# Optimization experiments

Measured on AMD Instinct MI355X. Metric: run time of the kernel, lower is better.

Reference implementation:

```python
import jax, jax.numpy as jnp
import numpy as np

N = 100000   # nodes
P = 3        # metapaths
E = 800000   # edges per metapath (avg degree 8)
IN = 128     # in_size
H = 4        # layer_num_heads
D = 32       # out_size per head
HID = 64     # semantic attention hidden
NEG_SLOPE = 0.2


def setup_inputs() -> dict:
    key = jax.random.key(0)
    ks = jax.random.split(key, 10)
    h = jax.random.normal(ks[0], (N, IN), jnp.float32)
    edge_src = jax.random.randint(ks[1], (P, E), 0, N, dtype=jnp.int32).astype(jnp.int64)
    edge_dst = jax.random.randint(ks[2], (P, E), 0, N, dtype=jnp.int32).astype(jnp.int64)
    W = jax.random.normal(ks[3], (P, IN, H * D), jnp.float32) * 0.05
    attn_l = jax.random.normal(ks[4], (P, H, D), jnp.float32) * 0.05
    attn_r = jax.random.normal(ks[5], (P, H, D), jnp.float32) * 0.05
    bias = jnp.zeros((P, H * D), jnp.float32)
    sa_w1 = jax.random.normal(ks[6], (H * D, HID), jnp.float32) * 0.05
    sa_b1 = jnp.zeros((HID,), jnp.float32)
    sa_w2 = jax.random.normal(ks[7], (HID, 1), jnp.float32) * 0.05
    return {"h": h, "edge_src": edge_src, "edge_dst": edge_dst, "W": W,
            "attn_l": attn_l, "attn_r": attn_r, "bias": bias,
            "sa_w1": sa_w1, "sa_b1": sa_b1, "sa_w2": sa_w2}


def _gat_conv(h, src, dst, Wp, al, ar, bp):
    # DGL GATConv: project, per-edge additive attention, edge softmax over dst, scatter-sum.
    n = h.shape[0]
    feat = (h @ Wp).reshape(n, H, D)              # [N,H,D]
    el = (feat * al).sum(-1)                      # [N,H]
    er = (feat * ar).sum(-1)                      # [N,H]
    e = jax.nn.leaky_relu(el[src] + er[dst], NEG_SLOPE)   # [E,H]
    emax = jax.ops.segment_max(e, dst, num_segments=n)    # [N,H]
    emax = jnp.where(jnp.isfinite(emax), emax, 0.0)       # zero-in-degree guard
    ex = jnp.exp(e - emax[dst])                            # [E,H]
    denom = jax.ops.segment_sum(ex, dst, num_segments=n)   # [N,H]
    alpha = ex / jnp.maximum(denom[dst], 1e-9)              # [E,H]
    msg = alpha[:, :, None] * feat[src]                     # [E,H,D]
    out = jax.ops.segment_sum(msg, dst, num_segments=n)     # [N,H,D]
    return out.reshape(n, H * D) + bp


def reference(h, edge_src, edge_dst, W, attn_l, attn_r, bias, sa_w1, sa_b1, sa_w2):
    embs = []
    for p in range(P):  # small fixed metapath set
        embs.append(_gat_conv(h, edge_src[p], edge_dst[p], W[p], attn_l[p], attn_r[p], bias[p]))
    z = jnp.stack(embs, axis=1)                 # [N,P,H*D]
    # SemanticAttention: MLP score, mean over nodes, softmax over metapaths
    w = (jnp.tanh(z @ sa_w1 + sa_b1) @ sa_w2).mean(0)   # [P,1]
    beta = jax.nn.softmax(w, axis=0)                     # [P,1]
    return (beta[None, :, :] * z).sum(1)                 # [N,H*D]
```

## Files before the change

kernel.cpp:

```cpp
#include <hip/hip_runtime.h>
#include <hip/hip_bf16.h>
#include <math.h>

#define NN 100000
#define NP 3
#define NE 800000
#define NH 4
#define ND 32
#define HD 128
#define NHID 64

#define SLW 256
#define SBK 512
#define GB 391
#define NBLK 196
#define ECHUNK 4096
#define EPT 16
#define EMAX 2560

typedef __attribute__((ext_vector_type(8))) short short8;
typedef __attribute__((ext_vector_type(4))) float f32x4;

__device__ __forceinline__ unsigned short f2bf(float f) {
  union { float f; unsigned int u; } v; v.f = f;
  unsigned int r = v.u + 0x7FFFu + ((v.u >> 16) & 1u);
  return (unsigned short)(r >> 16);
}
__device__ __forceinline__ float bf2f(unsigned short u) {
  return __uint_as_float(((unsigned int)u) << 16);
}
__device__ __forceinline__ float tanh_fast(float x) {
  return 1.f - 2.f / (1.f + __expf(2.f * x));
}

__global__ __launch_bounds__(256) void prep_fill_kernel(
    const float* __restrict__ h, const float* __restrict__ W, const float* __restrict__ W1,
    const int* __restrict__ src_all, const int* __restrict__ dst_all,
    unsigned short* __restrict__ hb, unsigned short* __restrict__ WT,
    unsigned short* __restrict__ W1T, float* __restrict__ s,
    int* __restrict__ cntA, int* __restrict__ baseA, int* __restrict__ pairs) {
  __shared__ int hist[SBK];
  __shared__ int scanb[SBK];
  const int tid = threadIdx.x;
  const int bx = blockIdx.x;
  if (bx < 12500) {
    int i = bx * 256 + tid;
    if (i < NN * 32) {
      float4 v = ((const float4*)h)[i];
      ushort4 o;
      o.x = f2bf(v.x); o.y = f2bf(v.y); o.z = f2bf(v.z); o.w = f2bf(v.w);
      ((ushort4*)hb)[i] = o;
    }
    if (i < NP * 128 * 128) {
      int p = i >> 14, r = i & 16383, n = r >> 7, k = r & 127;
      WT[i] = f2bf(W[(size_t)p * 16384 + k * 128 + n]);
    }
    if (i < NHID * 128) {
      int n = i >> 7, k = i & 127;
      W1T[i] = f2bf(W1[(size_t)k * NHID + n]);
    }
    if (i < 4) s[i] = 0.f;
    return;
  }
  const int b2 = bx - 12500;
  const int p = b2 / NBLK, blk = b2 % NBLK;
  const int* dstp = dst_all + (size_t)p * NE;
  const int* srcp = src_all + (size_t)p * NE;
  hist[tid] = 0; hist[tid + 256] = 0;
  __syncthreads();
  int dv[EPT], sv[EPT];
#pragma unroll
  for (int k = 0; k < EPT; ++k) {
    int e = blk * ECHUNK + k * 256 + tid;
    dv[k] = -1; sv[k] = 0;
    if (e < NE) {
      dv[k] = __builtin_nontemporal_load(dstp + e);
      sv[k] = __builtin_nontemporal_load(srcp + e);
    }
    if (dv[k] >= 0) atomicAdd(&hist[(unsigned)dv[k] >> 8], 1);
  }
  __syncthreads();
  scanb[tid] = hist[tid]; scanb[tid + 256] = hist[tid + 256];
  __syncthreads();
  for (int off = 1; off < SBK; off <<= 1) {
    int a0 = (tid >= off) ? scanb[tid - off] : 0;
    int a1 = scanb[tid + 256 - off];
    __syncthreads();
    scanb[tid] += a0; scanb[tid + 256] += a1;
    __syncthreads();
  }
  int c0 = hist[tid], c1 = hist[tid + 256];
  int b0 = scanb[tid] - c0, b1 = scanb[tid + 256] - c1;
  int* cA = cntA + ((size_t)p * NBLK + blk) * SBK;
  int* bA = baseA + ((size_t)p * NBLK + blk) * SBK;
  cA[tid] = c0; cA[tid + 256] = c1;
  bA[tid] = b0; bA[tid + 256] = b1;
  __syncthreads();
  scanb[tid] = b0; scanb[tid + 256] = b1;
  hist[tid] = 0; hist[tid + 256] = 0;
  __syncthreads();
  int* prp = pairs + (size_t)p * NE + (size_t)blk * ECHUNK;
#pragma unroll
  for (int k = 0; k < EPT; ++k) {
    if (dv[k] >= 0) {
      int sl = (unsigned)dv[k] >> 8;
      int pos = scanb[sl] + atomicAdd(&hist[sl], 1);
      prp[pos] = ((dv[k] & 255) << 17) | sv[k];
    }
  }
}

__global__ __launch_bounds__(256) void gemm_mfma_kernel(
    const unsigned short* __restrict__ hb, const unsigned short* __restrict__ WT_all,
    const float* __restrict__ al_all, const float* __restrict__ ar_all,
    unsigned short* __restrict__ featb_all, float* __restrict__ el_all,
    float* __restrict__ er_all) {
  __shared__ unsigned short Bs[128 * 128];
  const int p = blockIdx.y;
  const unsigned short* WTp = WT_all + (size_t)p * 16384;
#pragma unroll
  for (int it = 0; it < 8; ++it)
    ((float4*)Bs)[it * 256 + threadIdx.x] = ((const float4*)WTp)[it * 256 + threadIdx.x];
  __syncthreads();

  const int wid = threadIdx.x >> 6, lane = threadIdx.x & 63;
  const int c = lane & 15, q = lane >> 4;
  const int tile = blockIdx.x * 4 + wid;
  const int tc = tile < 6250 ? tile : 6249;

  f32x4 acc[8];
#pragma unroll
  for (int t = 0; t < 8; ++t) acc[t] = (f32x4){0.f, 0.f, 0.f, 0.f};

  const unsigned short* arow = hb + (size_t)(tc * 16 + c) * 128 + q * 8;
#pragma unroll
  for (int kc = 0; kc < 4; ++kc) {
    short8 a = *(const short8*)(arow + kc * 32);
#pragma unroll
    for (int t = 0; t < 8; ++t) {
      short8 b = *(const short8*)(Bs + (size_t)(t * 16 + c) * 128 + kc * 32 + q * 8);
      acc[t] = __builtin_amdgcn_mfma_f32_16x16x32_bf16(a, b, acc[t], 0, 0, 0);
    }
  }
  if (tile >= 6250) return;

  unsigned short* featb = featb_all + (size_t)p * NN * 128;
#pragma unroll
  for (int t = 0; t < 8; ++t)
#pragma unroll
    for (int i = 0; i < 4; ++i)
      featb[(size_t)(tc * 16 + q * 4 + i) * 128 + t * 16 + c] = f2bf(acc[t][i]);

  const float* al = al_all + p * 128;
  const float* ar = ar_all + p * 128;
  float alv[8], arv[8];
#pragma unroll
  for (int t = 0; t < 8; ++t) { alv[t] = al[t * 16 + c]; arv[t] = ar[t * 16 + c]; }
  float elp[4][4], erp[4][4];
#pragma unroll
  for (int i = 0; i < 4; ++i)
#pragma unroll
    for (int hh = 0; hh < 4; ++hh) {
      elp[i][hh] = acc[2 * hh][i] * alv[2 * hh] + acc[2 * hh + 1][i] * alv[2 * hh + 1];
      erp[i][hh] = acc[2 * hh][i] * arv[2 * hh] + acc[2 * hh + 1][i] * arv[2 * hh + 1];
    }
#pragma unroll
  for (int m = 1; m <= 8; m <<= 1)
#pragma unroll
    for (int i = 0; i < 4; ++i)
#pragma unroll
      for (int hh = 0; hh < 4; ++hh) {
        elp[i][hh] += __shfl_xor(elp[i][hh], m);
        erp[i][hh] += __shfl_xor(erp[i][hh], m);
      }
  if (c == 0) {
    float* el = el_all + (size_t)p * NN * 4;
    float* er = er_all + (size_t)p * NN * 4;
#pragma unroll
    for (int i = 0; i < 4; ++i) {
      int row = tc * 16 + q * 4 + i;
      *(float4*)(el + (size_t)row * 4) = make_float4(elp[i][0], elp[i][1], elp[i][2], elp[i][3]);
      *(float4*)(er + (size_t)row * 4) = make_float4(erp[i][0], erp[i][1], erp[i][2], erp[i][3]);
    }
  }
}

__global__ __launch_bounds__(512) void gather2_kernel(
    const unsigned short* __restrict__ featb_all, const float* __restrict__ el_all,
    const float* __restrict__ er_all, const int* __restrict__ cntA,
    const int* __restrict__ baseA, const int* __restrict__ pairs,
    const float* __restrict__ bias_all, unsigned short* __restrict__ zb) {
  __shared__ int scnt[NBLK];
  __shared__ int sbase[NBLK];
  __shared__ int scum[NBLK];
  __shared__ int totE;
  __shared__ int hist[SLW];
  __shared__ int start[SLW];
  __shared__ int wcur[SLW];
  __shared__ int earr[EMAX];
  __shared__ int srt[EMAX];
  const int tid = threadIdx.x;
  const int p = blockIdx.y, sl = blockIdx.x;

  for (int b = tid; b < NBLK; b += 512) {
    scnt[b] = cntA[((size_t)p * NBLK + b) * SBK + sl];
    sbase[b] = baseA[((size_t)p * NBLK + b) * SBK + sl];
  }
  if (tid < SLW) hist[tid] = 0;
  __syncthreads();
  if (tid < NBLK) scum[tid] = scnt[tid];
  __syncthreads();
  for (int off = 1; off < NBLK; off <<= 1) {
    int a = (tid < NBLK && tid >= off) ? scum[tid - off] : 0;
    __syncthreads();
    if (tid < NBLK) scum[tid] += a;
    __syncthreads();
  }
  if (tid == NBLK - 1) { int t = scum[NBLK - 1]; totE = t > EMAX ? EMAX : t; }
  int excl = (tid < NBLK) ? scum[tid] - scnt[tid] : 0;
  __syncthreads();
  if (tid < NBLK) scum[tid] = excl;
  __syncthreads();
  const int total = totE;
  const int* prp = pairs + (size_t)p * NE;
  for (int e = tid; e < total; e += 512) {
    int lo = 0, hi = NBLK - 1;
    while (lo < hi) { int mid = (lo + hi + 1) >> 1; if (scum[mid] <= e) lo = mid; else hi = mid - 1; }
    int pk = prp[(size_t)lo * ECHUNK + sbase[lo] + (e - scum[lo])];
    earr[e] = pk;
    atomicAdd(&hist[pk >> 17], 1);
  }
  __syncthreads();
  if (tid < SLW) start[tid] = hist[tid];
  __syncthreads();
  for (int off = 1; off < SLW; off <<= 1) {
    int a = (tid < SLW && tid >= off) ? start[tid - off] : 0;
    __syncthreads();
    if (tid < SLW) start[tid] += a;
    __syncthreads();
  }
  if (tid < SLW) { int st = start[tid] - hist[tid]; start[tid] = st; wcur[tid] = st; }
  __syncthreads();
  for (int e = tid; e < total; e += 512) {
    int pk = earr[e];
    int pos = atomicAdd(&wcur[pk >> 17], 1);
    srt[pos] = pk & 0x1FFFF;
  }
  __syncthreads();

  const unsigned short* featb = featb_all + (size_t)p * NN * 128;
  const float* el = el_all + (size_t)p * NN * 4;
  const int w = tid >> 6, lane = tid & 63;
  const int j16 = lane & 15, hgrp = lane >> 4;
  const int sub = lane >> 4, c16 = lane & 15;
  const int hh = c16 >> 2;
  for (int nl = w; nl < SLW; nl += 8) {
    int n = sl * SLW + nl;
    if (n >= NN) continue;
    int deg = hist[nl];
    int st = start[nl];
    float4 ern = *(const float4*)(er_all + (size_t)p * NN * 4 + (size_t)n * 4);
    const float ernh = hgrp == 0 ? ern.x : hgrp == 1 ? ern.y : hgrp == 2 ? ern.z : ern.w;
    float acc[8] = {0.f, 0.f, 0.f, 0.f, 0.f, 0.f, 0.f, 0.f};
    float dsum = 0.f;
    for (int b = 0; b < deg; b += 16) {
      int s = 0; float x = 0.f;
      int jj = b + j16;
      if (jj < deg) {
        s = srt[st + jj];
        float ev = el[(size_t)s * 4 + hgrp];
        float e = ev + ernh; e = fmaxf(e, 0.2f * e);
        x = __expf(e);
      }
      int bend = deg - b; bend = bend > 16 ? 16 : bend;
      for (int i = 0; i < bend; i += 8) {
        int j0 = i + sub, j1 = i + 4 + sub;
        int s0 = __shfl(s, j0);
        int s1 = __shfl(s, j1);
        float xv0 = __shfl(x, (hh << 4) | j0);
        float xv1 = __shfl(x, (hh << 4) | j1);
        short8 f0 = *(const short8*)(featb + (size_t)s0 * 128 + c16 * 8);
        short8 f1 = *(const short8*)(featb + (size_t)s1 * 128 + c16 * 8);
        dsum += xv0 + xv1;
#pragma unroll
        for (int k = 0; k < 8; ++k) acc[k] += xv0 * bf2f((unsigned short)f0[k]);
#pragma unroll
        for (int k = 0; k < 8; ++k) acc[k] += xv1 * bf2f((unsigned short)f1[k]);
      }
    }
    dsum += __shfl_xor(dsum, 16); dsum += __shfl_xor(dsum, 32);
#pragma unroll
    for (int k = 0; k < 8; ++k) {
      acc[k] += __shfl_xor(acc[k], 16);
      acc[k] += __shfl_xor(acc[k], 32);
    }
    if (sub == 0) {
      float rd = dsum > 0.f ? 1.f / dsum : 0.f;
      const float* bias = bias_all + p * 128 + c16 * 8;
      float4 b0 = *(const float4*)(bias);
      float4 b1 = *(const float4*)(bias + 4);
      short8 o;
      o[0] = f2bf(acc[0] * rd + b0.x); o[1] = f2bf(acc[1] * rd + b0.y);
      o[2] = f2bf(acc[2] * rd + b0.z); o[3] = f2bf(acc[3] * rd + b0.w);
      o[4] = f2bf(acc[4] * rd + b1.x); o[5] = f2bf(acc[5] * rd + b1.y);
      o[6] = f2bf(acc[6] * rd + b1.z); o[7] = f2bf(acc[7] * rd + b1.w);
      *(short8*)(zb + (size_t)n * (NP * 128) + p * 128 + c16 * 8) = o;
    }
  }
}

__global__ __launch_bounds__(256) void sem_mfma_kernel(
    const unsigned short* __restrict__ zb, const unsigned short* __restrict__ W1T,
    const float* __restrict__ b1, const float* __restrict__ w2,
    float* __restrict__ s) {
  __shared__ float red3[3];
  if (threadIdx.x < 3) red3[threadIdx.x] = 0.f;
  __syncthreads();
  const int wid = threadIdx.x >> 6, lane = threadIdx.x & 63;
  const int tile = blockIdx.x * 4 + wid;
  const bool active = tile < 18750;
  const int tc = active ? tile : 18749;
  const int c = lane & 15, q = lane >> 4;
  f32x4 acc[4];
#pragma unroll
  for (int t = 0; t < 4; ++t) acc[t] = (f32x4){0.f, 0.f, 0.f, 0.f};

  const unsigned short* arow = zb + (size_t)(tc * 16 + c) * 128 + q * 8;
  const unsigned short* brow = W1T + (size_t)c * 128 + q * 8;
#pragma unroll
  for (int kc = 0; kc < 4; ++kc) {
    short8 a = *(const short8*)(arow + kc * 32);
#pragma unroll
    for (int t = 0; t < 4; ++t) {
      short8 b = *(const short8*)(brow + (size_t)t * 16 * 128 + kc * 32);
      acc[t] = __builtin_amdgcn_mfma_f32_16x16x32_bf16(a, b, acc[t], 0, 0, 0);
    }
  }
  float part[4] = {0.f, 0.f, 0.f, 0.f};
#pragma unroll
  for (int t = 0; t < 4; ++t) {
    float bb = b1[t * 16 + c], ww = w2[t * 16 + c];
#pragma unroll
    for (int i = 0; i < 4; ++i) part[i] += tanh_fast(acc[t][i] + bb) * ww;
  }
#pragma unroll
  for (int m = 1; m <= 8; m <<= 1)
#pragma unroll
    for (int i = 0; i < 4; ++i) part[i] += __shfl_xor(part[i], m);
  if (active && c == 0) {
#pragma unroll
    for (int i = 0; i < 4; ++i)
      atomicAdd(&red3[(tc * 16 + q * 4 + i) % 3], part[i]);
  }
  __syncthreads();
  if (threadIdx.x < 3) atomicAdd(&s[threadIdx.x], red3[threadIdx.x]);
}

__global__ __launch_bounds__(256) void final_kernel(
    const unsigned short* __restrict__ zb, const float* __restrict__ s,
    float* __restrict__ out) {
  int i = blockIdx.x * blockDim.x + threadIdx.x;
  if (i >= NN * 16) return;
  float w0 = s[0] * (1.f / NN), w1 = s[1] * (1.f / NN), w2c = s[2] * (1.f / NN);
  float m = fmaxf(w0, fmaxf(w1, w2c));
  float e0 = __expf(w0 - m), e1 = __expf(w1 - m), e2 = __expf(w2c - m);
  float inv = 1.f / (e0 + e1 + e2);
  float b0 = e0 * inv, b1 = e1 * inv, b2 = e2 * inv;
  int n = i >> 4, g = i & 15;
  const unsigned short* zr = zb + (size_t)n * (NP * 128) + g * 8;
  ushort4 u0a = *(const ushort4*)(zr);
  ushort4 u0b = *(const ushort4*)(zr + 4);
  ushort4 u1a = *(const ushort4*)(zr + 128);
  ushort4 u1b = *(const ushort4*)(zr + 132);
  ushort4 u2a = *(const ushort4*)(zr + 256);
  ushort4 u2b = *(const ushort4*)(zr + 260);
  float4 oa, ob;
  oa.x = b0 * bf2f(u0a.x) + b1 * bf2f(u1a.x) + b2 * bf2f(u2a.x);
  oa.y = b0 * bf2f(u0a.y) + b1 * bf2f(u1a.y) + b2 * bf2f(u2a.y);
  oa.z = b0 * bf2f(u0a.z) + b1 * bf2f(u1a.z) + b2 * bf2f(u2a.z);
  oa.w = b0 * bf2f(u0a.w) + b1 * bf2f(u1a.w) + b2 * bf2f(u2a.w);
  ob.x = b0 * bf2f(u0b.x) + b1 * bf2f(u1b.x) + b2 * bf2f(u2b.x);
  ob.y = b0 * bf2f(u0b.y) + b1 * bf2f(u1b.y) + b2 * bf2f(u2b.y);
  ob.z = b0 * bf2f(u0b.z) + b1 * bf2f(u1b.z) + b2 * bf2f(u2b.z);
  ob.w = b0 * bf2f(u0b.w) + b1 * bf2f(u1b.w) + b2 * bf2f(u2b.w);
  float* op = out + (size_t)n * 128 + g * 8;
  *(float4*)op = oa;
  *(float4*)(op + 4) = ob;
}

extern "C" void kernel_launch(void* const* d_in, const int* in_sizes, int n_in,
                              void* d_out, int out_size, void* d_ws, size_t ws_size,
                              hipStream_t stream) {
  const float* h    = (const float*)d_in[0];
  const int*   esrc = (const int*)d_in[1];
  const int*   edst = (const int*)d_in[2];
  const float* W    = (const float*)d_in[3];
  const float* al   = (const float*)d_in[4];
  const float* ar   = (const float*)d_in[5];
  const float* bias = (const float*)d_in[6];
  const float* w1   = (const float*)d_in[7];
  const float* b1   = (const float*)d_in[8];
  const float* w2   = (const float*)d_in[9];
  float* out = (float*)d_out;

  unsigned short* zb    = (unsigned short*)d_ws;
  unsigned short* featb = zb + (size_t)38400000;
  unsigned short* WT    = featb + (size_t)38400000;
  unsigned short* W1T   = WT + 49152;
  float* el   = (float*)(W1T + 8192);
  float* er   = el + (size_t)NP * NN * 4;
  float* s    = er + (size_t)NP * NN * 4;
  int* cntA  = (int*)(s + 16);
  int* baseA = cntA + (size_t)NP * NBLK * SBK;
  int* pairs = baseA + (size_t)NP * NBLK * SBK;
  unsigned short* hb = (unsigned short*)(pairs + (size_t)NP * NE);

  prep_fill_kernel<<<12500 + NP * NBLK, 256, 0, stream>>>(
      h, W, w1, esrc, edst, hb, WT, W1T, s, cntA, baseA, pairs);

  dim3 gemmGrid(NN / 64 + 1, NP);
  gemm_mfma_kernel<<<gemmGrid, 256, 0, stream>>>(hb, WT, al, ar, featb, el, er);

  dim3 g2Grid(GB, NP);
  gather2_kernel<<<g2Grid, 512, 0, stream>>>(featb, el, er, cntA, baseA, pairs, bias, zb);

  sem_mfma_kernel<<<(18750 + 3) / 4, 256, 0, stream>>>(zb, W1T, b1, w2, s);
  final_kernel<<<(NN * 16 + 255) / 256, 256, 0, stream>>>(zb, s, out);
}
```

Before: 474.7 us.

## Split gather into CSR build, edge-weight precompute, and per-node gather kernels

The fused gather kernel, which bucket-sorted edges in shared memory and then aggregated, is split into three kernels. One builds per-slice sorted edge lists and row indices in global memory, one computes exp attention weights per edge for all heads, and one does the per-destination-node feature gather with one wave per node across a much larger grid. This removes the large shared-memory footprint that limited occupancy in the gather phase, and the CSR build is placed before the GEMM. In exchange it adds global-memory round trips for the sorted edges and weights, two extra launches, and a lower EMAX cap that could truncate edges in dense slices.

```diff
diff --git a/kernel.cpp b/kernel.cpp
--- a/kernel.cpp
+++ b/kernel.cpp
@@ -16,7 +16,7 @@
 #define NBLK 196
 #define ECHUNK 4096
 #define EPT 16
-#define EMAX 2560
+#define EMAX 2368
 
 typedef __attribute__((ext_vector_type(8))) short short8;
 typedef __attribute__((ext_vector_type(4))) float f32x4;
@@ -185,11 +185,10 @@
   }
 }
 
-__global__ __launch_bounds__(512) void gather2_kernel(
-    const unsigned short* __restrict__ featb_all, const float* __restrict__ el_all,
-    const float* __restrict__ er_all, const int* __restrict__ cntA,
-    const int* __restrict__ baseA, const int* __restrict__ pairs,
-    const float* __restrict__ bias_all, unsigned short* __restrict__ zb) {
+__global__ __launch_bounds__(512) void fillB2a_kernel(
+    const int* __restrict__ cntA, const int* __restrict__ baseA,
+    const int* __restrict__ pairs, int* __restrict__ srtpk,
+    int2* __restrict__ rowidx, int* __restrict__ btot) {
   __shared__ int scnt[NBLK];
   __shared__ int sbase[NBLK];
   __shared__ int scum[NBLK];
@@ -198,9 +197,9 @@
   __shared__ int start[SLW];
   __shared__ int wcur[SLW];
   __shared__ int earr[EMAX];
-  __shared__ int srt[EMAX];
   const int tid = threadIdx.x;
   const int p = blockIdx.y, sl = blockIdx.x;
+  const size_t base = ((size_t)p * GB + sl) * EMAX;
 
   for (int b = tid; b < NBLK; b += 512) {
     scnt[b] = cntA[((size_t)p * NBLK + b) * SBK + sl];
@@ -244,68 +243,99 @@
   for (int e = tid; e < total; e += 512) {
     int pk = earr[e];
     int pos = atomicAdd(&wcur[pk >> 17], 1);
-    srt[pos] = pk & 0x1FFFF;
-  }
-  __syncthreads();
-
+    srtpk[base + pos] = pk;
+  }
+  if (tid < SLW) {
+    int n = sl * SLW + tid;
+    if (n < NN) rowidx[(size_t)p * NN + n] = make_int2((int)(base + start[tid]), hist[tid]);
+  }
+  if (tid == 0) btot[p * GB + sl] = total;
+}
+
+__global__ __launch_bounds__(256) void fillB2b_kernel(
+    const int* __restrict__ srtpk, const int* __restrict__ btot,
+    const float* __restrict__ el_all, const float* __restrict__ er_all,
+    float4* __restrict__ xs) {
+  const int p = blockIdx.y, sl = blockIdx.x;
+  const int total = btot[p * GB + sl];
+  const size_t base = ((size_t)p * GB + sl) * EMAX;
+  const float* el = el_all + (size_t)p * NN * 4;
+  const float* er = er_all + (size_t)p * NN * 4;
+  for (int i = threadIdx.x; i < total; i += 256) {
+    int pk = srtpk[base + i];
+    int src = pk & 0x1FFFF, dl = pk >> 17;
+    int n = sl * SLW + dl;
+    float4 ev = *(const float4*)(el + (size_t)src * 4);
+    float4 rv = *(const float4*)(er + (size_t)n * 4);
+    float4 x;
+    float e0 = ev.x + rv.x; e0 = fmaxf(e0, 0.2f * e0); x.x = __expf(e0);
+    float e1 = ev.y + rv.y; e1 = fmaxf(e1, 0.2f * e1); x.y = __expf(e1);
+    float e2 = ev.z + rv.z; e2 = fmaxf(e2, 0.2f * e2); x.z = __expf(e2);
+    float e3 = ev.w + rv.w; e3 = fmaxf(e3, 0.2f * e3); x.w = __expf(e3);
+    xs[base + i] = x;
+  }
+}
+
+__global__ __launch_bounds__(256) void gather3_kernel(
+    const unsigned short* __restrict__ featb_all, const int* __restrict__ srtpk,
+    const float* __restrict__ xs, const int2* __restrict__ rowidx,
+    const float* __restrict__ bias_all, unsigned short* __restrict__ zb) {
+  const int p = blockIdx.y;
   const unsigned short* featb = featb_all + (size_t)p * NN * 128;
-  const float* el = el_all + (size_t)p * NN * 4;
-  const int w = tid >> 6, lane = tid & 63;
+  const int wid = threadIdx.x >> 6;
+  const int lane = threadIdx.x & 63;
+  const int n = blockIdx.x * 4 + wid;
+  int2 rd = rowidx[(size_t)p * NN + n];
+  const int rbase = rd.x, deg = rd.y;
+
   const int j16 = lane & 15, hgrp = lane >> 4;
   const int sub = lane >> 4, c16 = lane & 15;
   const int hh = c16 >> 2;
-  for (int nl = w; nl < SLW; nl += 8) {
-    int n = sl * SLW + nl;
-    if (n >= NN) continue;
-    int deg = hist[nl];
-    int st = start[nl];
-    float4 ern = *(const float4*)(er_all + (size_t)p * NN * 4 + (size_t)n * 4);
-    const float ernh = hgrp == 0 ? ern.x : hgrp == 1 ? ern.y : hgrp == 2 ? ern.z : ern.w;
-    float acc[8] = {0.f, 0.f, 0.f, 0.f, 0.f, 0.f, 0.f, 0.f};
-    float dsum = 0.f;
-    for (int b = 0; b < deg; b += 16) {
-      int s = 0; float x = 0.f;
-      int jj = b + j16;
-      if (jj < deg) {
-        s = srt[st + jj];
-        float ev = el[(size_t)s * 4 + hgrp];
-        float e = ev + ernh; e = fmaxf(e, 0.2f * e);
-        x = __expf(e);
-      }
-      int bend = deg - b; bend = bend > 16 ? 16 : bend;
-      for (int i = 0; i < bend; i += 8) {
-        int j0 = i + sub, j1 = i + 4 + sub;
-        int s0 = __shfl(s, j0);
-        int s1 = __shfl(s, j1);
-        float xv0 = __shfl(x, (hh << 4) | j0);
-        float xv1 = __shfl(x, (hh << 4) | j1);
-        short8 f0 = *(const short8*)(featb + (size_t)s0 * 128 + c16 * 8);
-        short8 f1 = *(const short8*)(featb + (size_t)s1 * 128 + c16 * 8);
-        dsum += xv0 + xv1;
-#pragma unroll
-        for (int k = 0; k < 8; ++k) acc[k] += xv0 * bf2f((unsigned short)f0[k]);
-#pragma unroll
-        for (int k = 0; k < 8; ++k) acc[k] += xv1 * bf2f((unsigned short)f1[k]);
-      }
-    }
-    dsum += __shfl_xor(dsum, 16); dsum += __shfl_xor(dsum, 32);
-#pragma unroll
-    for (int k = 0; k < 8; ++k) {
-      acc[k] += __shfl_xor(acc[k], 16);
-      acc[k] += __shfl_xor(acc[k], 32);
-    }
-    if (sub == 0) {
-      float rd = dsum > 0.f ? 1.f / dsum : 0.f;
-      const float* bias = bias_all + p * 128 + c16 * 8;
-      float4 b0 = *(const float4*)(bias);
-      float4 b1 = *(const float4*)(bias + 4);
-      short8 o;
-      o[0] = f2bf(acc[0] * rd + b0.x); o[1] = f2bf(acc[1] * rd + b0.y);
-      o[2] = f2bf(acc[2] * rd + b0.z); o[3] = f2bf(acc[3] * rd + b0.w);
-      o[4] = f2bf(acc[4] * rd + b1.x); o[5] = f2bf(acc[5] * rd + b1.y);
-      o[6] = f2bf(acc[6] * rd + b1.z); o[7] = f2bf(acc[7] * rd + b1.w);
-      *(short8*)(zb + (size_t)n * (NP * 128) + p * 128 + c16 * 8) = o;
-    }
+
+  float acc[8] = {0.f, 0.f, 0.f, 0.f, 0.f, 0.f, 0.f, 0.f};
+  float dsum = 0.f;
+
+  for (int b = 0; b < deg; b += 16) {
+    int s = 0; float x = 0.f;
+    int jj = b + j16;
+    if (jj < deg) {
+      int idx = rbase + jj;
+      s = srtpk[idx] & 0x1FFFF;
+      x = xs[(size_t)idx * 4 + hgrp];
+    }
+    int bend = deg - b; bend = bend > 16 ? 16 : bend;
+    for (int i = 0; i < bend; i += 8) {
+      int j0 = i + sub, j1 = i + 4 + sub;
+      int s0 = __shfl(s, j0);
+      int s1 = __shfl(s, j1);
+      float xv0 = __shfl(x, (hh << 4) | j0);
+      float xv1 = __shfl(x, (hh << 4) | j1);
+      short8 f0 = *(const short8*)(featb + (size_t)s0 * 128 + c16 * 8);
+      short8 f1 = *(const short8*)(featb + (size_t)s1 * 128 + c16 * 8);
+      dsum += xv0 + xv1;
+#pragma unroll
+      for (int k = 0; k < 8; ++k) acc[k] += xv0 * bf2f((unsigned short)f0[k]);
+#pragma unroll
+      for (int k = 0; k < 8; ++k) acc[k] += xv1 * bf2f((unsigned short)f1[k]);
+    }
+  }
+  dsum += __shfl_xor(dsum, 16); dsum += __shfl_xor(dsum, 32);
+#pragma unroll
+  for (int k = 0; k < 8; ++k) {
+    acc[k] += __shfl_xor(acc[k], 16);
+    acc[k] += __shfl_xor(acc[k], 32);
+  }
+  if (sub == 0) {
+    float rdn = dsum > 0.f ? 1.f / dsum : 0.f;
+    const float* bias = bias_all + p * 128 + c16 * 8;
+    float4 b0 = *(const float4*)(bias);
+    float4 b1 = *(const float4*)(bias + 4);
+    short8 o;
+    o[0] = f2bf(acc[0] * rdn + b0.x); o[1] = f2bf(acc[1] * rdn + b0.y);
+    o[2] = f2bf(acc[2] * rdn + b0.z); o[3] = f2bf(acc[3] * rdn + b0.w);
+    o[4] = f2bf(acc[4] * rdn + b1.x); o[5] = f2bf(acc[5] * rdn + b1.y);
+    o[6] = f2bf(acc[6] * rdn + b1.z); o[7] = f2bf(acc[7] * rdn + b1.w);
+    *(short8*)(zb + (size_t)n * (NP * 128) + p * 128 + c16 * 8) = o;
   }
 }
 
@@ -408,21 +438,30 @@
   unsigned short* WT    = featb + (size_t)38400000;
   unsigned short* W1T   = WT + 49152;
   float* el   = (float*)(W1T + 8192);
-  float* er   = el + (size_t)NP * NN * 4;
-  float* s    = er + (size_t)NP * NN * 4;
-  int* cntA  = (int*)(s + 16);
+  float* er   = el + (size_t)1200000;
+  float* s    = er + (size_t)1200000;
+  int2* rowidx = (int2*)(s + 16);
+  int* btot  = (int*)(rowidx + (size_t)NP * NN);
+  int* srtpk = btot + 1280;
+  int* cntA  = srtpk + (size_t)NP * GB * EMAX;
   int* baseA = cntA + (size_t)NP * NBLK * SBK;
   int* pairs = baseA + (size_t)NP * NBLK * SBK;
   unsigned short* hb = (unsigned short*)(pairs + (size_t)NP * NE);
+  float* xs = (float*)cntA;
 
   prep_fill_kernel<<<12500 + NP * NBLK, 256, 0, stream>>>(
       h, W, w1, esrc, edst, hb, WT, W1T, s, cntA, baseA, pairs);
 
+  dim3 bGrid(GB, NP);
+  fillB2a_kernel<<<bGrid, 512, 0, stream>>>(cntA, baseA, pairs, srtpk, rowidx, btot);
+
   dim3 gemmGrid(NN / 64 + 1, NP);
   gemm_mfma_kernel<<<gemmGrid, 256, 0, stream>>>(hb, WT, al, ar, featb, el, er);
 
-  dim3 g2Grid(GB, NP);
-  gather2_kernel<<<g2Grid, 512, 0, stream>>>(featb, el, er, cntA, baseA, pairs, bias, zb);
+  fillB2b_kernel<<<bGrid, 256, 0, stream>>>(srtpk, btot, el, er, (float4*)xs);
+
+  dim3 gatherGrid(NN / 4, NP);
+  gather3_kernel<<<gatherGrid, 256, 0, stream>>>(featb, srtpk, xs, rowidx, bias, zb);
 
   sem_mfma_kernel<<<(18750 + 3) / 4, 256, 0, stream>>>(zb, W1T, b1, w2, s);
   final_kernel<<<(NN * 16 + 255) / 256, 256, 0, stream>>>(zb, s, out);
```

New measurement: 457.5 us. -3.6%, faster.
